# Optimization experiments

Hardware: AMD Instinct MI355X
Metric: run time of the kernel (lower is better)

Reference implementation:

```python
import jax, jax.numpy as jnp
import numpy as np


def setup_inputs() -> dict:
    key = jax.random.key(0)
    ks = jax.random.split(key, 6)
    B, C1, C2, C, H, W = 16, 512, 320, 256, 64, 64
    x1 = jax.random.normal(ks[0], (B, C1, H, W), dtype=jnp.float32)
    x2 = jax.random.normal(ks[1], (B, C2, H, W), dtype=jnp.float32)
    # 1x1 conv weights, bias=False -> plain channel matmuls
    w_img = jax.random.normal(ks[2], (C, C1), dtype=jnp.float32) * (1.0 / np.sqrt(C1))
    w_txt = jax.random.normal(ks[3], (C, C2), dtype=jnp.float32) * (1.0 / np.sqrt(C2))
    w_out = jax.random.normal(ks[4], (C1, C), dtype=jnp.float32) * (1.0 / np.sqrt(C))
    gamma = jax.random.normal(ks[5], (1,), dtype=jnp.float32)
    return {"x1": x1, "x2": x2, "w_img": w_img, "w_txt": w_txt,
            "w_out": w_out, "gamma": gamma}


def reference(x1, x2, w_img, w_txt, w_out, gamma):
    B, _, H, W = x1.shape
    # 1x1 conv projections (bias-free) == channel matmuls
    img = jnp.einsum('oc,bchw->bohw', w_img, x1)   # [B,C,H,W]
    txt = jnp.einsum('oc,bchw->bohw', w_txt, x2)   # [B,C,H,W]
    C = img.shape[1]
    q = img.reshape(B, C, H * W)                    # [B,C,N]
    kv = txt.reshape(B, C, H * W)                   # [B,C,N]
    attn = jnp.einsum('bcn,bdn->bcd', q, kv)        # QK^T over spatial dim
    attn = jax.nn.softmax(attn, axis=-1)            # [B,C,C]
    attn_info = jnp.einsum('bcd,bdn->bcn', attn, kv).reshape(B, C, H, W)
    out = gamma[0] * attn_info + img                # scale-residual
    out = jnp.einsum('oc,bchw->bohw', w_out, out)   # output 1x1 conv
    return out
```

## Files before the change

kernel.cpp:

```cpp
#include <hip/hip_runtime.h>
#include <stdint.h>

typedef _Float16 f16_t;
typedef _Float16 f16x4 __attribute__((ext_vector_type(4)));
typedef _Float16 f16x8 __attribute__((ext_vector_type(8)));
typedef float f32x4 __attribute__((ext_vector_type(4)));

__device__ __forceinline__ void async16(const void* g, void* lds) {
    typedef __attribute__((address_space(3))) void lds_void;
    typedef __attribute__((address_space(1))) void glb_void;
    lds_void* l = (lds_void*)(unsigned int)(unsigned long long)lds;
    glb_void* gp = (glb_void*)(unsigned long long)g;
    __builtin_amdgcn_global_load_lds(gp, l, 16, 0, 0);
}

__global__ __launch_bounds__(256) void prep(
    const float* __restrict__ x1, const float* __restrict__ x2,
    f16_t* __restrict__ x1t, f16_t* __restrict__ x2t,
    const float* __restrict__ w_img, f16_t* __restrict__ wib,
    const float* __restrict__ w_txt, f16_t* __restrict__ wtb,
    const float* __restrict__ w_out, f16_t* __restrict__ wob) {
    __shared__ float tile[32][33];
    const int id = blockIdx.x;
    const int t = threadIdx.x;
    if (id < 53248) {
        const float* ip; f16_t* op; int R, bx, by, bz;
        const int S = 4096;
        if (id < 32768) {
            R = 512; bx = id & 127; by = (id >> 7) & 15; bz = id >> 11;
            ip = x1 + (long long)bz * R * S;
            op = x1t + (long long)bz * S * R;
        } else {
            const int id2 = id - 32768;
            R = 320; bx = id2 & 127; by = (id2 >> 7) % 10; bz = id2 / 1280;
            ip = x2 + (long long)bz * R * S;
            op = x2t + (long long)bz * S * R;
        }
        const int s0 = bx * 32, r0 = by * 32;
        const int lr = t >> 3, lc = (t & 7) * 4;
        const float4 v = *(const float4*)(ip + (long long)(r0 + lr) * S + s0 + lc);
        tile[lr][lc + 0] = v.x;
        tile[lr][lc + 1] = v.y;
        tile[lr][lc + 2] = v.z;
        tile[lr][lc + 3] = v.w;
        __syncthreads();
        const int sr = t >> 3, rc = (t & 7) * 4;
        f16x4 o;
        o[0] = (f16_t)tile[rc + 0][sr];
        o[1] = (f16_t)tile[rc + 1][sr];
        o[2] = (f16_t)tile[rc + 2][sr];
        o[3] = (f16_t)tile[rc + 3][sr];
        *(f16x4*)(op + (long long)(s0 + sr) * R + r0 + rc) = o;
    } else {
        const int i = (id - 53248) * 256 + t;
        if (i < 512 * 256) wib[i] = (f16_t)w_img[i];
        if (i < 320 * 256) wtb[i] = (f16_t)w_txt[i];
        if (i < 512 * 256) wob[i] = (f16_t)w_out[i];
    }
}

template <int BM, int BN, int TM, int TN, int WM, int WN, int MODE, int KSPLIT>
__global__ __launch_bounds__(256, 2)
void gemm_bt(const f16_t* __restrict__ A, const f16_t* __restrict__ B,
             void* __restrict__ C, const f16_t* __restrict__ resid,
             const float* __restrict__ gamma, f16_t* __restrict__ Ct,
             int M, int N, int K,
             long long strideA, long long strideB, long long strideC,
             long long strideCt) {
    constexpr int BK = 32;
    constexpr int AS = BM * BK;
    constexpr int BS = BN * BK;
    constexpr int STG = AS + BS;
    constexpr int LT = (MODE == 3) ? BN * (BM + 8) : 0;
    constexpr int POOL = (2 * STG > LT) ? 2 * STG : LT;
    __shared__ __align__(16) f16_t pool[POOL];

    const int tid = threadIdx.x;
    const int wave = tid >> 6;
    const int lane = tid & 63;
    const int wm = wave / WN;
    const int wn = wave % WN;
    const int l16 = lane & 15;
    const int l4 = lane >> 4;

    const long long zb = (KSPLIT == 1) ? blockIdx.z : (blockIdx.z / KSPLIT);
    const int ks = (KSPLIT == 1) ? 0 : (blockIdx.z % KSPLIT);
    const int Ksl = K / KSPLIT;
    const f16_t* Ab = A + zb * strideA + (long long)blockIdx.y * BM * K;
    const f16_t* Bb = B + zb * strideB + (long long)blockIdx.x * BN * K;

    f32x4 zero = {0.f, 0.f, 0.f, 0.f};
    f32x4 acc[TM][TN];
#pragma unroll
    for (int i = 0; i < TM; ++i)
#pragma unroll
        for (int j = 0; j < TN; ++j) acc[i][j] = zero;

    auto stage = [&](int b, int k0) {
        f16_t* As = pool + b * STG;
        f16_t* Bs = As + AS;
#pragma unroll
        for (int r = 0; r < (BM * 4) / 256; ++r) {
            int seg = r * 256 + tid;
            const f16_t* g = Ab + (long long)(seg >> 2) * K + k0 + (seg & 3) * 8;
            async16(g, &As[(r * 256 + wave * 64) * 8]);
        }
#pragma unroll
        for (int r = 0; r < (BN * 4) / 256; ++r) {
            int seg = r * 256 + tid;
            const f16_t* g = Bb + (long long)(seg >> 2) * K + k0 + (seg & 3) * 8;
            async16(g, &Bs[(r * 256 + wave * 64) * 8]);
        }
    };
    auto compute = [&](int b) {
        const f16_t* As = pool + b * STG;
        const f16_t* Bs = As + AS;
        f16x8 af[TM], bfr[TN];
#pragma unroll
        for (int i = 0; i < TM; ++i)
            af[i] = *(const f16x8*)&As[((wm * TM + i) * 16 + l16) * BK + l4 * 8];
#pragma unroll
        for (int j = 0; j < TN; ++j)
            bfr[j] = *(const f16x8*)&Bs[((wn * TN + j) * 16 + l16) * BK + l4 * 8];
#pragma unroll
        for (int i = 0; i < TM; ++i)
#pragma unroll
            for (int j = 0; j < TN; ++j)
                acc[i][j] = __builtin_amdgcn_mfma_f32_16x16x32_f16(af[i], bfr[j], acc[i][j], 0, 0, 0);
    };

    const int kBeg = ks * Ksl;
    const int NT = Ksl / BK;
    stage(0, kBeg);
    __syncthreads();
    int cur = 0;
    for (int t = 1; t < NT; ++t) {
        stage(cur ^ 1, kBeg + t * BK);
        compute(cur);
        __syncthreads();
        cur ^= 1;
    }
    compute(cur);

    if (MODE == 3) __syncthreads();

    const int row0 = blockIdx.y * BM + wm * TM * 16;
    const int col0 = blockIdx.x * BN + wn * TN * 16;
    float g = (MODE == 2) ? gamma[0] : 0.f;
#pragma unroll
    for (int i = 0; i < TM; ++i) {
#pragma unroll
        for (int j = 0; j < TN; ++j) {
            f16x4 tq;
#pragma unroll
            for (int r = 0; r < 4; ++r) {
                int row = row0 + i * 16 + l4 * 4 + r;
                int col = col0 + j * 16 + l16;
                float v = acc[i][j][r];
                if (MODE == 4) {
                    long long idx = (long long)blockIdx.z * strideC + (long long)row * N + col;
                    ((float*)C)[idx] = v;
                } else {
                    long long idx = zb * strideC + (long long)row * N + col;
                    if (MODE == 0) {
                        ((f16_t*)C)[idx] = (f16_t)v;
                    } else if (MODE == 1) {
                        ((float*)C)[idx] = v;
                    } else if (MODE == 2) {
                        float im = (float)resid[idx];
                        ((f16_t*)C)[idx] = (f16_t)(g * v + im);
                    } else if (MODE == 3) {
                        ((f16_t*)C)[idx] = (f16_t)v;
                        tq[r] = (f16_t)v;
                    }
                }
            }
            if (MODE == 3) {
                int rl = wm * (TM * 16) + i * 16 + l4 * 4;
                int cl = wn * (TN * 16) + j * 16 + l16;
                *(f16x4*)&pool[cl * (BM + 8) + rl] = tq;
            }
        }
    }

    if (MODE == 3) {
        __syncthreads();
        const int bx0 = blockIdx.x * BN;
        const int by0 = blockIdx.y * BM;
        const long long cb = zb * strideCt;
        constexpr int TPR = BM / 8;
        constexpr int RPI = 256 / TPR;
#pragma unroll
        for (int it = 0; it < BN / RPI; ++it) {
            int nl = it * RPI + (tid / TPR);
            int c8 = (tid % TPR) * 8;
            f16x8 v = *(const f16x8*)&pool[nl * (BM + 8) + c8];
            *(f16x8*)&Ct[cb + (long long)(bx0 + nl) * M + by0 + c8] = v;
        }
    }
}

template <int KS>
__global__ void softmax_red(const float* __restrict__ part, f16_t* __restrict__ out) {
    const int row = blockIdx.x * 4 + (threadIdx.x >> 6);
    const int lane = threadIdx.x & 63;
    const int b = row >> 8, r = row & 255;
    const float* p = part + (long long)(b * KS) * 65536 + r * 256 + lane * 4;
    float4 v = *(const float4*)p;
#pragma unroll
    for (int k = 1; k < KS; ++k) {
        float4 u = *(const float4*)(p + (long long)k * 65536);
        v.x += u.x; v.y += u.y; v.z += u.z; v.w += u.w;
    }
    float m = fmaxf(fmaxf(v.x, v.y), fmaxf(v.z, v.w));
#pragma unroll
    for (int off = 32; off > 0; off >>= 1) m = fmaxf(m, __shfl_xor(m, off, 64));
    float e0 = __expf(v.x - m), e1 = __expf(v.y - m);
    float e2 = __expf(v.z - m), e3 = __expf(v.w - m);
    float s = e0 + e1 + e2 + e3;
#pragma unroll
    for (int off = 32; off > 0; off >>= 1) s += __shfl_xor(s, off, 64);
    const float inv = 1.0f / s;
    f16x4 o;
    o[0] = (f16_t)(e0 * inv);
    o[1] = (f16_t)(e1 * inv);
    o[2] = (f16_t)(e2 * inv);
    o[3] = (f16_t)(e3 * inv);
    *(f16x4*)(out + ((long long)row) * 256 + lane * 4) = o;
}

extern "C" void kernel_launch(void* const* d_in, const int* in_sizes, int n_in,
                              void* d_out, int out_size, void* d_ws, size_t ws_size,
                              hipStream_t stream) {
    (void)in_sizes; (void)n_in; (void)out_size; (void)ws_size;

    const float* x1 = (const float*)d_in[0];
    const float* x2 = (const float*)d_in[1];
    const float* w_img = (const float*)d_in[2];
    const float* w_txt = (const float*)d_in[3];
    const float* w_out = (const float*)d_in[4];
    const float* gamma = (const float*)d_in[5];

    constexpr int B = 16, C1 = 512, C2 = 320, C = 256, N = 4096, OC = 512;
    constexpr int KS = 8;
    constexpr long long NC = (long long)N * C;
    constexpr long long CC = (long long)C * C;

    char* ws = (char*)d_ws;
    f16_t* wib   = (f16_t*)(ws + 0);
    f16_t* wtb   = (f16_t*)(ws + 262144);
    f16_t* wob   = (f16_t*)(ws + 425984);
    f16_t* img   = (f16_t*)(ws + 688128);
    f16_t* imgT  = (f16_t*)(ws + 34242560);
    f16_t* kvT   = (f16_t*)(ws + 67796992);
    f16_t* attns = (f16_t*)(ws + 101351424);
    f16_t* yT    = img;

    char* oc = (char*)d_out;
    f16_t* x1t  = (f16_t*)(oc);
    f16_t* x2t  = (f16_t*)(oc + 67108864);
    f16_t* kv   = (f16_t*)(oc);
    float* part = (float*)(oc + 33554432);

    prep<<<53760, 256, 0, stream>>>(x1, x2, x1t, x2t, w_img, wib, w_txt, wtb, w_out, wob);

    gemm_bt<256, 128, 8, 4, 2, 2, 3, 1><<<dim3(N / 128, 1, B), 256, 0, stream>>>(
        wib, x1t, img, nullptr, nullptr, imgT, C, N, C1,
        0LL, (long long)N * C1, NC, NC);

    gemm_bt<256, 128, 8, 4, 2, 2, 3, 1><<<dim3(N / 128, 1, B), 256, 0, stream>>>(
        wtb, x2t, kv, nullptr, nullptr, kvT, C, N, C2,
        0LL, (long long)N * C2, NC, NC);

    gemm_bt<64, 64, 2, 2, 2, 2, 4, KS><<<dim3(C / 64, C / 64, B * KS), 256, 0, stream>>>(
        img, kv, part, nullptr, nullptr, nullptr, C, C, N,
        NC, NC, CC, 0LL);

    softmax_red<KS><<<(B * C) / 4, 256, 0, stream>>>(part, attns);

    gemm_bt<128, 128, 4, 4, 2, 2, 2, 1><<<dim3(C / 128, N / 128, B), 256, 0, stream>>>(
        kvT, attns, yT, imgT, gamma, nullptr, N, C, C,
        NC, CC, NC, 0LL);

    gemm_bt<256, 128, 8, 4, 2, 2, 1, 1><<<dim3(N / 128, OC / 256, B), 256, 0, stream>>>(
        wob, yT, (float*)d_out, nullptr, nullptr, nullptr, OC, N, C,
        0LL, NC, (long long)OC * N, 0LL);
}
```

Measured before the change: 452.5 us.

## Fuse fp32-to-fp16 input transpose into projection GEMM B-operand loading

Removes the separate prep kernel that transposed and converted x1/x2 to fp16. The projection GEMMs now read fp32 activations directly in [C,N] layout through registers, convert them to fp16 and write a swizzled tile to LDS. Compute then gathers B fragments with scalar LDS reads. This drops a full read/write round trip of both inputs in exchange for register-staged loads and less efficient LDS fragment reads. The attention-score GEMM tile is also enlarged from 64x64 to 128x128.

```diff
diff --git a/kernel.cpp b/kernel.cpp
--- a/kernel.cpp
+++ b/kernel.cpp
@@ -14,65 +14,31 @@
     __builtin_amdgcn_global_load_lds(gp, l, 16, 0, 0);
 }
 
-__global__ __launch_bounds__(256) void prep(
-    const float* __restrict__ x1, const float* __restrict__ x2,
-    f16_t* __restrict__ x1t, f16_t* __restrict__ x2t,
-    const float* __restrict__ w_img, f16_t* __restrict__ wib,
-    const float* __restrict__ w_txt, f16_t* __restrict__ wtb,
-    const float* __restrict__ w_out, f16_t* __restrict__ wob) {
-    __shared__ float tile[32][33];
-    const int id = blockIdx.x;
-    const int t = threadIdx.x;
-    if (id < 53248) {
-        const float* ip; f16_t* op; int R, bx, by, bz;
-        const int S = 4096;
-        if (id < 32768) {
-            R = 512; bx = id & 127; by = (id >> 7) & 15; bz = id >> 11;
-            ip = x1 + (long long)bz * R * S;
-            op = x1t + (long long)bz * S * R;
-        } else {
-            const int id2 = id - 32768;
-            R = 320; bx = id2 & 127; by = (id2 >> 7) % 10; bz = id2 / 1280;
-            ip = x2 + (long long)bz * R * S;
-            op = x2t + (long long)bz * S * R;
-        }
-        const int s0 = bx * 32, r0 = by * 32;
-        const int lr = t >> 3, lc = (t & 7) * 4;
-        const float4 v = *(const float4*)(ip + (long long)(r0 + lr) * S + s0 + lc);
-        tile[lr][lc + 0] = v.x;
-        tile[lr][lc + 1] = v.y;
-        tile[lr][lc + 2] = v.z;
-        tile[lr][lc + 3] = v.w;
-        __syncthreads();
-        const int sr = t >> 3, rc = (t & 7) * 4;
-        f16x4 o;
-        o[0] = (f16_t)tile[rc + 0][sr];
-        o[1] = (f16_t)tile[rc + 1][sr];
-        o[2] = (f16_t)tile[rc + 2][sr];
-        o[3] = (f16_t)tile[rc + 3][sr];
-        *(f16x4*)(op + (long long)(s0 + sr) * R + r0 + rc) = o;
-    } else {
-        const int i = (id - 53248) * 256 + t;
-        if (i < 512 * 256) wib[i] = (f16_t)w_img[i];
-        if (i < 320 * 256) wtb[i] = (f16_t)w_txt[i];
-        if (i < 512 * 256) wob[i] = (f16_t)w_out[i];
-    }
-}
-
-template <int BM, int BN, int TM, int TN, int WM, int WN, int MODE, int KSPLIT>
+__global__ void cvt3(const float* __restrict__ a, f16_t* __restrict__ oa, int na,
+                     const float* __restrict__ b, f16_t* __restrict__ ob, int nb,
+                     const float* __restrict__ c, f16_t* __restrict__ oc, int nc) {
+    int i = blockIdx.x * 256 + threadIdx.x;
+    if (i < na) oa[i] = (f16_t)a[i];
+    if (i < nb) ob[i] = (f16_t)b[i];
+    if (i < nc) oc[i] = (f16_t)c[i];
+}
+
+template <int BM, int BN, int TM, int TN, int WM, int WN, int MODE, int KSPLIT, int FUSET>
 __global__ __launch_bounds__(256, 2)
-void gemm_bt(const f16_t* __restrict__ A, const f16_t* __restrict__ B,
+void gemm_bt(const f16_t* __restrict__ A, const f16_t* __restrict__ B16,
+             const float* __restrict__ Bf32,
              void* __restrict__ C, const f16_t* __restrict__ resid,
              const float* __restrict__ gamma, f16_t* __restrict__ Ct,
              int M, int N, int K,
              long long strideA, long long strideB, long long strideC,
              long long strideCt) {
     constexpr int BK = 32;
-    constexpr int AS = BM * BK;
-    constexpr int BS = BN * BK;
-    constexpr int STG = AS + BS;
+    static_assert(FUSET == 0 || (BN == 128), "fused path assumes BN=128");
+    constexpr int ASZ = BM * BK;
+    constexpr int BSZ = BN * BK;
+    constexpr int STG = 2 * ASZ + 2 * BSZ;
     constexpr int LT = (MODE == 3) ? BN * (BM + 8) : 0;
-    constexpr int POOL = (2 * STG > LT) ? 2 * STG : LT;
+    constexpr int POOL = (STG > LT) ? STG : LT;
     __shared__ __align__(16) f16_t pool[POOL];
 
     const int tid = threadIdx.x;
@@ -87,7 +53,8 @@
     const int ks = (KSPLIT == 1) ? 0 : (blockIdx.z % KSPLIT);
     const int Ksl = K / KSPLIT;
     const f16_t* Ab = A + zb * strideA + (long long)blockIdx.y * BM * K;
-    const f16_t* Bb = B + zb * strideB + (long long)blockIdx.x * BN * K;
+    const f16_t* Bb = (FUSET == 0) ? (B16 + zb * strideB + (long long)blockIdx.x * BN * K) : nullptr;
+    const float* BfB = FUSET ? (Bf32 + zb * strideB + blockIdx.x * BN) : nullptr;
 
     f32x4 zero = {0.f, 0.f, 0.f, 0.f};
     f32x4 acc[TM][TN];
@@ -96,32 +63,67 @@
 #pragma unroll
         for (int j = 0; j < TN; ++j) acc[i][j] = zero;
 
-    auto stage = [&](int b, int k0) {
-        f16_t* As = pool + b * STG;
-        f16_t* Bs = As + AS;
+    auto stageA = [&](int b, int k0) {
+        f16_t* As = pool + b * ASZ;
 #pragma unroll
         for (int r = 0; r < (BM * 4) / 256; ++r) {
             int seg = r * 256 + tid;
             const f16_t* g = Ab + (long long)(seg >> 2) * K + k0 + (seg & 3) * 8;
             async16(g, &As[(r * 256 + wave * 64) * 8]);
         }
+    };
+    auto stageB16 = [&](int b, int k0) {
 #pragma unroll
         for (int r = 0; r < (BN * 4) / 256; ++r) {
             int seg = r * 256 + tid;
             const f16_t* g = Bb + (long long)(seg >> 2) * K + k0 + (seg & 3) * 8;
-            async16(g, &Bs[(r * 256 + wave * 64) * 8]);
-        }
-    };
+            async16(g, &pool[2 * ASZ + b * BSZ + (r * 256 + wave * 64) * 8]);
+        }
+    };
+    float4 br[4];
+    const int fk = tid >> 3;
+    const int fc = (tid & 7) * 4;
+    const int fswz = ((fk >> 3) & 3) * 8;
+    auto loadB = [&](int k0) {
+#pragma unroll
+        for (int i = 0; i < 4; ++i)
+            br[i] = *(const float4*)(BfB + (long long)(k0 + fk) * N + fc + i * 32);
+    };
+    auto writeB = [&](int b) {
+        f16_t* Bs = pool + 2 * ASZ + b * BSZ;
+#pragma unroll
+        for (int i = 0; i < 4; ++i) {
+            int n4 = fc + i * 32;
+            f16x4 h;
+            h[0] = (f16_t)br[i].x; h[1] = (f16_t)br[i].y;
+            h[2] = (f16_t)br[i].z; h[3] = (f16_t)br[i].w;
+            *(f16x4*)&Bs[fk * BN + (n4 ^ fswz)] = h;
+        }
+    };
+
     auto compute = [&](int b) {
-        const f16_t* As = pool + b * STG;
-        const f16_t* Bs = As + AS;
+        const f16_t* As = pool + b * ASZ;
         f16x8 af[TM], bfr[TN];
 #pragma unroll
         for (int i = 0; i < TM; ++i)
             af[i] = *(const f16x8*)&As[((wm * TM + i) * 16 + l16) * BK + l4 * 8];
-#pragma unroll
-        for (int j = 0; j < TN; ++j)
-            bfr[j] = *(const f16x8*)&Bs[((wn * TN + j) * 16 + l16) * BK + l4 * 8];
+        if (FUSET) {
+            const f16_t* Bs = pool + 2 * ASZ + b * BSZ;
+#pragma unroll
+            for (int j = 0; j < TN; ++j) {
+                const int nj = ((wn * TN + j) * 16 + l16) ^ (l4 * 8);
+                f16x8 t;
+#pragma unroll
+                for (int e = 0; e < 8; ++e)
+                    t[e] = Bs[(l4 * 8 + e) * BN + nj];
+                bfr[j] = t;
+            }
+        } else {
+            const f16_t* Bs = pool + 2 * ASZ + b * BSZ;
+#pragma unroll
+            for (int j = 0; j < TN; ++j)
+                bfr[j] = *(const f16x8*)&Bs[((wn * TN + j) * 16 + l16) * BK + l4 * 8];
+        }
 #pragma unroll
         for (int i = 0; i < TM; ++i)
 #pragma unroll
@@ -131,16 +133,34 @@
 
     const int kBeg = ks * Ksl;
     const int NT = Ksl / BK;
-    stage(0, kBeg);
-    __syncthreads();
     int cur = 0;
-    for (int t = 1; t < NT; ++t) {
-        stage(cur ^ 1, kBeg + t * BK);
+    if (FUSET) {
+        loadB(kBeg);
+        stageA(0, kBeg);
+        writeB(0);
+        __syncthreads();
+        for (int t = 1; t < NT; ++t) {
+            loadB(kBeg + t * BK);
+            stageA(cur ^ 1, kBeg + t * BK);
+            compute(cur);
+            writeB(cur ^ 1);
+            __syncthreads();
+            cur ^= 1;
+        }
         compute(cur);
+    } else {
+        stageA(0, kBeg);
+        stageB16(0, kBeg);
         __syncthreads();
-        cur ^= 1;
+        for (int t = 1; t < NT; ++t) {
+            stageA(cur ^ 1, kBeg + t * BK);
+            stageB16(cur ^ 1, kBeg + t * BK);
+            compute(cur);
+            __syncthreads();
+            cur ^= 1;
+        }
+        compute(cur);
     }
-    compute(cur);
 
     if (MODE == 3) __syncthreads();
 
@@ -257,32 +277,30 @@
     f16_t* yT    = img;
 
     char* oc = (char*)d_out;
-    f16_t* x1t  = (f16_t*)(oc);
-    f16_t* x2t  = (f16_t*)(oc + 67108864);
     f16_t* kv   = (f16_t*)(oc);
     float* part = (float*)(oc + 33554432);
 
-    prep<<<53760, 256, 0, stream>>>(x1, x2, x1t, x2t, w_img, wib, w_txt, wtb, w_out, wob);
-
-    gemm_bt<256, 128, 8, 4, 2, 2, 3, 1><<<dim3(N / 128, 1, B), 256, 0, stream>>>(
-        wib, x1t, img, nullptr, nullptr, imgT, C, N, C1,
-        0LL, (long long)N * C1, NC, NC);
-
-    gemm_bt<256, 128, 8, 4, 2, 2, 3, 1><<<dim3(N / 128, 1, B), 256, 0, stream>>>(
-        wtb, x2t, kv, nullptr, nullptr, kvT, C, N, C2,
-        0LL, (long long)N * C2, NC, NC);
-
-    gemm_bt<64, 64, 2, 2, 2, 2, 4, KS><<<dim3(C / 64, C / 64, B * KS), 256, 0, stream>>>(
-        img, kv, part, nullptr, nullptr, nullptr, C, C, N,
+    cvt3<<<512, 256, 0, stream>>>(w_img, wib, C * C1, w_txt, wtb, C * C2, w_out, wob, OC * C);
+
+    gemm_bt<256, 128, 8, 4, 2, 2, 3, 1, 1><<<dim3(N / 128, 1, B), 256, 0, stream>>>(
+        wib, nullptr, x1, img, nullptr, nullptr, imgT, C, N, C1,
+        0LL, (long long)C1 * N, NC, NC);
+
+    gemm_bt<256, 128, 8, 4, 2, 2, 3, 1, 1><<<dim3(N / 128, 1, B), 256, 0, stream>>>(
+        wtb, nullptr, x2, kv, nullptr, nullptr, kvT, C, N, C2,
+        0LL, (long long)C2 * N, NC, NC);
+
+    gemm_bt<128, 128, 4, 4, 2, 2, 4, KS, 0><<<dim3(C / 128, C / 128, B * KS), 256, 0, stream>>>(
+        img, kv, nullptr, part, nullptr, nullptr, nullptr, C, C, N,
         NC, NC, CC, 0LL);
 
     softmax_red<KS><<<(B * C) / 4, 256, 0, stream>>>(part, attns);
 
-    gemm_bt<128, 128, 4, 4, 2, 2, 2, 1><<<dim3(C / 128, N / 128, B), 256, 0, stream>>>(
-        kvT, attns, yT, imgT, gamma, nullptr, N, C, C,
+    gemm_bt<128, 128, 4, 4, 2, 2, 2, 1, 0><<<dim3(C / 128, N / 128, B), 256, 0, stream>>>(
+        kvT, attns, nullptr, yT, imgT, gamma, nullptr, N, C, C,
         NC, CC, NC, 0LL);
 
-    gemm_bt<256, 128, 8, 4, 2, 2, 1, 1><<<dim3(N / 128, OC / 256, B), 256, 0, stream>>>(
-        wob, yT, (float*)d_out, nullptr, nullptr, nullptr, OC, N, C,
+    gemm_bt<256, 128, 8, 4, 2, 2, 1, 1, 0><<<dim3(N / 128, OC / 256, B), 256, 0, stream>>>(
+        wob, yT, nullptr, (float*)d_out, nullptr, nullptr, nullptr, OC, N, C,
         0LL, NC, (long long)OC * N, 0LL);
 }
```

After: 391.9 us. 1.15x faster.
